# Kernel tuning notes

Hardware: AMD Instinct MI355X
Metric: run time of the kernel (lower is better)

The kernel has to match this reference:

```python
import jax, jax.numpy as jnp
import numpy as np

OUT, IN = 5632, 2048
GROUP_SIZE = 128
N_GROUPS = (OUT * IN) // GROUP_SIZE
LORA_SCALE = 32.0 / 16.0  # lora_alpha / lora_r


def dequantize_int4(packed, scales, zeros):
    # packed: [numel//2], each byte holds two 4-bit codes (low nibble first)
    low = packed & 0xF
    high = (packed >> 4) & 0xF
    q = jnp.stack([low, high], axis=-1).reshape(-1).astype(jnp.float32)  # [numel]
    q = q.reshape(N_GROUPS, GROUP_SIZE)
    w = (q - zeros[:, None]) * scales[:, None]
    return w.reshape(OUT, IN)


def setup_inputs() -> dict:
    key = jax.random.key(0)
    k1, k2, k3, k4, k5, k6 = jax.random.split(key, 6)
    x = jax.random.normal(k1, (4, 2048, IN), dtype=jnp.float32)
    packed = jax.random.randint(k2, ((OUT * IN) // 2,), 0, 256, dtype=jnp.int32)
    scales = jax.random.uniform(k3, (N_GROUPS,), dtype=jnp.float32) * 0.02 + 1e-3
    zeros = jax.random.uniform(k4, (N_GROUPS,), dtype=jnp.float32) * 15.0
    lora_A = jax.random.normal(k5, (IN, 16), dtype=jnp.float32) * (1.0 / np.sqrt(IN))
    lora_B = jax.random.normal(k6, (16, OUT), dtype=jnp.float32) * 0.02
    return {"x": x, "packed": packed, "scales": scales, "zeros": zeros,
            "lora_A": lora_A, "lora_B": lora_B}


def reference(x, packed, scales, zeros, lora_A, lora_B):
    W = dequantize_int4(packed, scales, zeros)            # [OUT, IN]
    base = jnp.einsum('bsi,oi->bso', x, W)                # F.linear(x, W)
    lora = ((x @ lora_A) @ lora_B) * LORA_SCALE           # low-rank path
    return base + lora
```

## Files before the change

### kernel.cpp

```cpp
#include <hip/hip_runtime.h>

#define M_DIM 8192
#define K_DIM 2048
#define N_DIM 5632

typedef __attribute__((ext_vector_type(8))) short short8;
typedef __attribute__((ext_vector_type(4))) short s4v;
typedef __attribute__((ext_vector_type(4))) float f32x4;

__device__ __forceinline__ short f2b(float f) {
  union { float f; unsigned u; } v; v.f = f;
  unsigned r = v.u + 0x7FFFu + ((v.u >> 16) & 1u);
  return (short)(r >> 16);
}

__device__ __forceinline__ void async16(void* lds, const void* g) {
  __builtin_amdgcn_global_load_lds(
      (const __attribute__((address_space(1))) unsigned*)g,
      (__attribute__((address_space(3))) unsigned*)lds,
      16, 0, 0);
}

__global__ __launch_bounds__(256) void cvt_x_kernel(const float* __restrict__ x,
                                                    short* __restrict__ xb) {
  long t = (long)blockIdx.x * 256 + threadIdx.x;
  float4 f = ((const float4*)x)[t];
  s4v o;
  o[0] = f2b(f.x); o[1] = f2b(f.y); o[2] = f2b(f.z); o[3] = f2b(f.w);
  *(s4v*)(xb + 4 * t) = o;
}

__global__ __launch_bounds__(256) void lat_kernel(const float* __restrict__ lA,
                                                  float* __restrict__ lAT) {
  int i = blockIdx.x * 256 + threadIdx.x;
  const float4* row = (const float4*)(lA + (size_t)i * 16);
  float4 v0 = row[0], v1 = row[1], v2 = row[2], v3 = row[3];
  float vals[16] = {v0.x, v0.y, v0.z, v0.w, v1.x, v1.y, v1.z, v1.w,
                    v2.x, v2.y, v2.z, v2.w, v3.x, v3.y, v3.z, v3.w};
#pragma unroll
  for (int r = 0; r < 16; ++r) lAT[r * K_DIM + i] = vals[r] * 2.0f;
}

__global__ __launch_bounds__(256) void dequant_lora_kernel(
    const int* __restrict__ packed, const float* __restrict__ scales,
    const float* __restrict__ zeros, const float* __restrict__ lAT,
    const float* __restrict__ lB, short* __restrict__ wb) {
  int o = blockIdx.x;
  int i0 = threadIdx.x * 8;
  long e0 = (long)o * K_DIM + i0;
  int4 p = ((const int4*)packed)[e0 >> 3];
  int g = (int)(e0 >> 7);
  float s = scales[g], z = zeros[g];

  float accv[8];
#pragma unroll
  for (int d = 0; d < 4; ++d) {
    int pv = (&p.x)[d];
    accv[2 * d]     = ((float)(pv & 0xF) - z) * s;
    accv[2 * d + 1] = ((float)((pv >> 4) & 0xF) - z) * s;
  }
#pragma unroll
  for (int r = 0; r < 16; ++r) {
    float b = lB[r * N_DIM + o];
    const float4* ar = (const float4*)&lAT[r * K_DIM + i0];
    float4 a0 = ar[0], a1 = ar[1];
    accv[0] += a0.x * b; accv[1] += a0.y * b;
    accv[2] += a0.z * b; accv[3] += a0.w * b;
    accv[4] += a1.x * b; accv[5] += a1.y * b;
    accv[6] += a1.z * b; accv[7] += a1.w * b;
  }
  short8 out8;
#pragma unroll
  for (int j = 0; j < 8; ++j) out8[j] = f2b(accv[j]);
  *(short8*)(wb + e0) = out8;
}

__global__ __launch_bounds__(512, 2) void gemm_kernel(const short* __restrict__ xb,
                                                      const short* __restrict__ wb,
                                                      float* __restrict__ out) {
  __shared__ __align__(16) short lds[65536];

  const int tid = threadIdx.x;
  const int lane = tid & 63;
  const int wave = tid >> 6;
  const int wm = wave >> 2, wn = wave & 3;
  const int l15 = lane & 15, quad = lane >> 4;

  int flat = blockIdx.x;
  int swz = (flat & 7) * 88 + (flat >> 3);
  int bm = swz / 22, bn = swz - bm * 22;
  const int m0 = bm * 256, n0 = bn * 256;

  const short* a_base = xb + (size_t)m0 * K_DIM;
  const short* b_base = wb + (size_t)n0 * K_DIM;

  const int rswz = quad ^ ((l15 >> 1) & 3);
  const int a_rd = (wm * 128 + l15) * 32 + rswz * 8;
  const int b_rd = 32768 + (wn * 64 + l15) * 32 + rswz * 8;

  const int srow = tid >> 2;
  const int schunk = (tid & 3) ^ ((srow >> 1) & 3);
  const short* ag0 = a_base + (size_t)srow * K_DIM + schunk * 8;
  const short* ag1 = ag0 + (size_t)128 * K_DIM;
  const short* bg0 = b_base + (size_t)srow * K_DIM + schunk * 8;
  const short* bg1 = bg0 + (size_t)128 * K_DIM;
  const int sl0 = tid * 8, sl1 = (512 + tid) * 8;

  f32x4 acc[8][4] = {};
  short8 bfA[4], af1A[4], bfB[4], af1B[4];

#pragma unroll
  for (int t = 0; t < 3; ++t) {
    const int sb = t * 8192;
    async16(&lds[sb + sl0], ag0 + t * 32);
    async16(&lds[sb + sl1], ag1 + t * 32);
    async16(&lds[32768 + sb + sl0], bg0 + t * 32);
    async16(&lds[32768 + sb + sl1], bg1 + t * 32);
  }
  asm volatile("s_waitcnt vmcnt(4)" ::: "memory");
  __builtin_amdgcn_s_barrier();
#pragma unroll
  for (int ni = 0; ni < 4; ++ni) bfA[ni] = *(const short8*)&lds[b_rd + ni * 512];
#pragma unroll
  for (int mi = 0; mi < 4; ++mi) af1A[mi] = *(const short8*)&lds[a_rd + mi * 512];

  auto tile = [&](int k, short8* bfc, short8* af1c, short8* bfn, short8* af1n,
                  bool do_stage, bool do_pref) {
    const int bo = (k & 3) * 8192;
    const int no_ = ((k + 1) & 3) * 8192;
    const int so = ((k + 3) & 3) * 8192;
    short8 af2[4];
#pragma unroll
    for (int mi = 0; mi < 4; ++mi)
      af2[mi] = *(const short8*)&lds[bo + a_rd + (4 + mi) * 512];
    if (do_pref) {
#pragma unroll
      for (int ni = 0; ni < 4; ++ni)
        bfn[ni] = *(const short8*)&lds[no_ + b_rd + ni * 512];
#pragma unroll
      for (int mi = 0; mi < 4; ++mi)
        af1n[mi] = *(const short8*)&lds[no_ + a_rd + mi * 512];
    }
    if (do_stage) {
      async16(&lds[so + sl0], ag0 + (k + 3) * 32);
      async16(&lds[so + sl1], ag1 + (k + 3) * 32);
      async16(&lds[32768 + so + sl0], bg0 + (k + 3) * 32);
      async16(&lds[32768 + so + sl1], bg1 + (k + 3) * 32);
    }
    __builtin_amdgcn_s_setprio(1);
#pragma unroll
    for (int mi = 0; mi < 4; ++mi)
#pragma unroll
      for (int ni = 0; ni < 4; ++ni)
        acc[mi][ni] = __builtin_amdgcn_mfma_f32_16x16x32_bf16(
            af1c[mi], bfc[ni], acc[mi][ni], 0, 0, 0);
#pragma unroll
    for (int mi = 0; mi < 4; ++mi)
#pragma unroll
      for (int ni = 0; ni < 4; ++ni)
        acc[4 + mi][ni] = __builtin_amdgcn_mfma_f32_16x16x32_bf16(
            af2[mi], bfc[ni], acc[4 + mi][ni], 0, 0, 0);
    __builtin_amdgcn_s_setprio(0);
  };

#pragma unroll 1
  for (int k = 0; k < 60; k += 2) {
    tile(k, bfA, af1A, bfB, af1B, true, true);
    asm volatile("s_waitcnt vmcnt(4)" ::: "memory");
    __builtin_amdgcn_s_barrier();
    tile(k + 1, bfB, af1B, bfA, af1A, true, true);
    asm volatile("s_waitcnt vmcnt(4)" ::: "memory");
    __builtin_amdgcn_s_barrier();
  }
  tile(60, bfA, af1A, bfB, af1B, true, true);
  asm volatile("s_waitcnt vmcnt(4)" ::: "memory");
  __builtin_amdgcn_s_barrier();
  tile(61, bfB, af1B, bfA, af1A, false, true);
  asm volatile("s_waitcnt vmcnt(0)" ::: "memory");
  __builtin_amdgcn_s_barrier();
  tile(62, bfA, af1A, bfB, af1B, false, true);
  tile(63, bfB, af1B, bfA, af1A, false, false);

  float* op = out + (size_t)(m0 + wm * 128 + quad * 4) * N_DIM + n0 + wn * 64 + l15;
#pragma unroll
  for (int mi = 0; mi < 8; ++mi)
#pragma unroll
    for (int r = 0; r < 4; ++r)
#pragma unroll
      for (int ni = 0; ni < 4; ++ni)
        op[(size_t)(mi * 16 + r) * N_DIM + ni * 16] = acc[mi][ni][r];
}

extern "C" void kernel_launch(void* const* d_in, const int* in_sizes, int n_in,
                              void* d_out, int out_size, void* d_ws, size_t ws_size,
                              hipStream_t stream) {
  const float* x      = (const float*)d_in[0];
  const int*   packed = (const int*)d_in[1];
  const float* scales = (const float*)d_in[2];
  const float* zeros  = (const float*)d_in[3];
  const float* lA     = (const float*)d_in[4];
  const float* lB     = (const float*)d_in[5];
  float* out = (float*)d_out;

  short* xb = (short*)d_ws;
  short* wb = xb + (size_t)M_DIM * K_DIM;
  float* lAT = out + ((size_t)4 * 2048 * N_DIM - 16 * K_DIM);

  cvt_x_kernel<<<(M_DIM * K_DIM) / (256 * 4), 256, 0, stream>>>(x, xb);
  lat_kernel<<<K_DIM / 256, 256, 0, stream>>>(lA, lAT);
  dequant_lora_kernel<<<N_DIM, 256, 0, stream>>>(packed, scales, zeros, lAT, lB, wb);
  gemm_kernel<<<dim3(N_DIM / 256 * (M_DIM / 256)), 512, 0, stream>>>(xb, wb, out);
}
```

Measured before the change: 456.9 us.

## Split GEMM k-tile into four barrier-separated phases with interleaved fragment loads

```diff
diff --git a/kernel.cpp b/kernel.cpp
--- a/kernel.cpp
+++ b/kernel.cpp
@@ -88,8 +88,8 @@
 
   int flat = blockIdx.x;
   int swz = (flat & 7) * 88 + (flat >> 3);
-  int bm = swz / 22, bn = swz - bm * 22;
-  const int m0 = bm * 256, n0 = bn * 256;
+  int bm = swz / 22, bn_ = swz - bm * 22;
+  const int m0 = bm * 256, n0 = bn_ * 256;
 
   const short* a_base = xb + (size_t)m0 * K_DIM;
   const short* b_base = wb + (size_t)n0 * K_DIM;
@@ -107,7 +107,7 @@
   const int sl0 = tid * 8, sl1 = (512 + tid) * 8;
 
   f32x4 acc[8][4] = {};
-  short8 bfA[4], af1A[4], bfB[4], af1B[4];
+  short8 bfA[4], bfB[4], aX[2], aY[2];
 
 #pragma unroll
   for (int t = 0; t < 3; ++t) {
@@ -121,65 +121,81 @@
   __builtin_amdgcn_s_barrier();
 #pragma unroll
   for (int ni = 0; ni < 4; ++ni) bfA[ni] = *(const short8*)&lds[b_rd + ni * 512];
-#pragma unroll
-  for (int mi = 0; mi < 4; ++mi) af1A[mi] = *(const short8*)&lds[a_rd + mi * 512];
-
-  auto tile = [&](int k, short8* bfc, short8* af1c, short8* bfn, short8* af1n,
-                  bool do_stage, bool do_pref) {
+  aX[0] = *(const short8*)&lds[a_rd];
+  aX[1] = *(const short8*)&lds[a_rd + 512];
+
+  auto tile = [&](int k, short8* bc, short8* bnx, bool do_stage, bool do_next,
+                  int vm) {
     const int bo = (k & 3) * 8192;
     const int no_ = ((k + 1) & 3) * 8192;
     const int so = ((k + 3) & 3) * 8192;
-    short8 af2[4];
-#pragma unroll
-    for (int mi = 0; mi < 4; ++mi)
-      af2[mi] = *(const short8*)&lds[bo + a_rd + (4 + mi) * 512];
-    if (do_pref) {
-#pragma unroll
-      for (int ni = 0; ni < 4; ++ni)
-        bfn[ni] = *(const short8*)&lds[no_ + b_rd + ni * 512];
-#pragma unroll
-      for (int mi = 0; mi < 4; ++mi)
-        af1n[mi] = *(const short8*)&lds[no_ + a_rd + mi * 512];
-    }
-    if (do_stage) {
-      async16(&lds[so + sl0], ag0 + (k + 3) * 32);
-      async16(&lds[so + sl1], ag1 + (k + 3) * 32);
-      async16(&lds[32768 + so + sl0], bg0 + (k + 3) * 32);
-      async16(&lds[32768 + so + sl1], bg1 + (k + 3) * 32);
-    }
-    __builtin_amdgcn_s_setprio(1);
-#pragma unroll
-    for (int mi = 0; mi < 4; ++mi)
-#pragma unroll
-      for (int ni = 0; ni < 4; ++ni)
-        acc[mi][ni] = __builtin_amdgcn_mfma_f32_16x16x32_bf16(
-            af1c[mi], bfc[ni], acc[mi][ni], 0, 0, 0);
-#pragma unroll
-    for (int mi = 0; mi < 4; ++mi)
-#pragma unroll
-      for (int ni = 0; ni < 4; ++ni)
-        acc[4 + mi][ni] = __builtin_amdgcn_mfma_f32_16x16x32_bf16(
-            af2[mi], bfc[ni], acc[4 + mi][ni], 0, 0, 0);
-    __builtin_amdgcn_s_setprio(0);
+    aY[0] = *(const short8*)&lds[bo + a_rd + 2 * 512];
+    aY[1] = *(const short8*)&lds[bo + a_rd + 3 * 512];
+    if (do_stage) async16(&lds[so + sl0], ag0 + (k + 3) * 32);
+    __builtin_amdgcn_s_setprio(1);
+#pragma unroll
+    for (int ni = 0; ni < 4; ++ni) {
+      acc[0][ni] = __builtin_amdgcn_mfma_f32_16x16x32_bf16(aX[0], bc[ni], acc[0][ni], 0, 0, 0);
+      acc[1][ni] = __builtin_amdgcn_mfma_f32_16x16x32_bf16(aX[1], bc[ni], acc[1][ni], 0, 0, 0);
+    }
+    __builtin_amdgcn_s_setprio(0);
+    __builtin_amdgcn_s_barrier();
+    aX[0] = *(const short8*)&lds[bo + a_rd + 4 * 512];
+    aX[1] = *(const short8*)&lds[bo + a_rd + 5 * 512];
+    if (do_next) {
+      bnx[0] = *(const short8*)&lds[no_ + b_rd];
+      bnx[1] = *(const short8*)&lds[no_ + b_rd + 512];
+    }
+    if (do_stage) async16(&lds[so + sl1], ag1 + (k + 3) * 32);
+    __builtin_amdgcn_s_setprio(1);
+#pragma unroll
+    for (int ni = 0; ni < 4; ++ni) {
+      acc[2][ni] = __builtin_amdgcn_mfma_f32_16x16x32_bf16(aY[0], bc[ni], acc[2][ni], 0, 0, 0);
+      acc[3][ni] = __builtin_amdgcn_mfma_f32_16x16x32_bf16(aY[1], bc[ni], acc[3][ni], 0, 0, 0);
+    }
+    __builtin_amdgcn_s_setprio(0);
+    __builtin_amdgcn_s_barrier();
+    aY[0] = *(const short8*)&lds[bo + a_rd + 6 * 512];
+    aY[1] = *(const short8*)&lds[bo + a_rd + 7 * 512];
+    if (do_next) {
+      bnx[2] = *(const short8*)&lds[no_ + b_rd + 2 * 512];
+      bnx[3] = *(const short8*)&lds[no_ + b_rd + 3 * 512];
+    }
+    if (do_stage) async16(&lds[32768 + so + sl0], bg0 + (k + 3) * 32);
+    __builtin_amdgcn_s_setprio(1);
+#pragma unroll
+    for (int ni = 0; ni < 4; ++ni) {
+      acc[4][ni] = __builtin_amdgcn_mfma_f32_16x16x32_bf16(aX[0], bc[ni], acc[4][ni], 0, 0, 0);
+      acc[5][ni] = __builtin_amdgcn_mfma_f32_16x16x32_bf16(aX[1], bc[ni], acc[5][ni], 0, 0, 0);
+    }
+    __builtin_amdgcn_s_setprio(0);
+    __builtin_amdgcn_s_barrier();
+    if (do_next) {
+      aX[0] = *(const short8*)&lds[no_ + a_rd];
+      aX[1] = *(const short8*)&lds[no_ + a_rd + 512];
+    }
+    if (do_stage) async16(&lds[32768 + so + sl1], bg1 + (k + 3) * 32);
+    __builtin_amdgcn_s_setprio(1);
+#pragma unroll
+    for (int ni = 0; ni < 4; ++ni) {
+      acc[6][ni] = __builtin_amdgcn_mfma_f32_16x16x32_bf16(aY[0], bc[ni], acc[6][ni], 0, 0, 0);
+      acc[7][ni] = __builtin_amdgcn_mfma_f32_16x16x32_bf16(aY[1], bc[ni], acc[7][ni], 0, 0, 0);
+    }
+    __builtin_amdgcn_s_setprio(0);
+    if (vm == 4) asm volatile("s_waitcnt vmcnt(4)" ::: "memory");
+    else if (vm == 0) asm volatile("s_waitcnt vmcnt(0)" ::: "memory");
+    __builtin_amdgcn_s_barrier();
   };
 
 #pragma unroll 1
   for (int k = 0; k < 60; k += 2) {
-    tile(k, bfA, af1A, bfB, af1B, true, true);
-    asm volatile("s_waitcnt vmcnt(4)" ::: "memory");
-    __builtin_amdgcn_s_barrier();
-    tile(k + 1, bfB, af1B, bfA, af1A, true, true);
-    asm volatile("s_waitcnt vmcnt(4)" ::: "memory");
-    __builtin_amdgcn_s_barrier();
-  }
-  tile(60, bfA, af1A, bfB, af1B, true, true);
-  asm volatile("s_waitcnt vmcnt(4)" ::: "memory");
-  __builtin_amdgcn_s_barrier();
-  tile(61, bfB, af1B, bfA, af1A, false, true);
-  asm volatile("s_waitcnt vmcnt(0)" ::: "memory");
-  __builtin_amdgcn_s_barrier();
-  tile(62, bfA, af1A, bfB, af1B, false, true);
-  tile(63, bfB, af1B, bfA, af1A, false, false);
+    tile(k,     bfA, bfB, true, true, 4);
+    tile(k + 1, bfB, bfA, true, true, 4);
+  }
+  tile(60, bfA, bfB, true,  true, 4);
+  tile(61, bfB, bfA, false, true, 0);
+  tile(62, bfA, bfB, false, true, -1);
+  tile(63, bfB, bfA, false, false, -1);
 
   float* op = out + (size_t)(m0 + wm * 128 + quad * 4) * N_DIM + n0 + wn * 64 + l15;
 #pragma unroll
@@ -188,7 +204,8 @@
     for (int r = 0; r < 4; ++r)
 #pragma unroll
       for (int ni = 0; ni < 4; ++ni)
-        op[(size_t)(mi * 16 + r) * N_DIM + ni * 16] = acc[mi][ni][r];
+        __builtin_nontemporal_store(acc[mi][ni][r],
+                                    &op[(size_t)(mi * 16 + r) * N_DIM + ni * 16]);
 }
 
 extern "C" void kernel_launch(void* const* d_in, const int* in_sizes, int n_in,
```

Result: no change. 455.6 us (-0.3%).

## Restructure GEMM main loop into double-buffered half-tile stages with staggered A/B loads

Applied to the files above, without the earlier changes.

```diff
diff --git a/kernel.cpp b/kernel.cpp
--- a/kernel.cpp
+++ b/kernel.cpp
@@ -88,98 +88,111 @@
 
   int flat = blockIdx.x;
   int swz = (flat & 7) * 88 + (flat >> 3);
-  int bm = swz / 22, bn = swz - bm * 22;
-  const int m0 = bm * 256, n0 = bn * 256;
+  int bm = swz / 22, bn_ = swz - bm * 22;
+  const int m0 = bm * 256, n0 = bn_ * 256;
 
   const short* a_base = xb + (size_t)m0 * K_DIM;
   const short* b_base = wb + (size_t)n0 * K_DIM;
 
-  const int rswz = quad ^ ((l15 >> 1) & 3);
-  const int a_rd = (wm * 128 + l15) * 32 + rswz * 8;
-  const int b_rd = 32768 + (wn * 64 + l15) * 32 + rswz * 8;
-
-  const int srow = tid >> 2;
-  const int schunk = (tid & 3) ^ ((srow >> 1) & 3);
-  const short* ag0 = a_base + (size_t)srow * K_DIM + schunk * 8;
-  const short* ag1 = ag0 + (size_t)128 * K_DIM;
-  const short* bg0 = b_base + (size_t)srow * K_DIM + schunk * 8;
-  const short* bg1 = bg0 + (size_t)128 * K_DIM;
+  const int a_rd = (wm * 128 + l15) * 32 + quad * 8;
+  const int b_rd = (wn * 64 + l15) * 32 + quad * 8;
+
+  const short* ag0 = a_base + (size_t)(tid >> 2) * K_DIM + (tid & 3) * 8;
+  const short* bg0 = b_base + (size_t)(tid >> 2) * K_DIM + (tid & 3) * 8;
   const int sl0 = tid * 8, sl1 = (512 + tid) * 8;
 
   f32x4 acc[8][4] = {};
-  short8 bfA[4], af1A[4], bfB[4], af1B[4];
-
-#pragma unroll
-  for (int t = 0; t < 3; ++t) {
-    const int sb = t * 8192;
-    async16(&lds[sb + sl0], ag0 + t * 32);
-    async16(&lds[sb + sl1], ag1 + t * 32);
-    async16(&lds[32768 + sb + sl0], bg0 + t * 32);
-    async16(&lds[32768 + sb + sl1], bg1 + t * 32);
-  }
+
+  auto stageA = [&](int t, int s) {
+    const int d = (t & 1) * 16384 + s * 8192;
+    const short* g = ag0 + t * 64 + s * 32;
+    async16(&lds[d + sl0], g);
+    async16(&lds[d + sl1], g + (size_t)128 * K_DIM);
+  };
+  auto stageB = [&](int t, int s) {
+    const int d = 32768 + (t & 1) * 16384 + s * 8192;
+    const short* g = bg0 + t * 64 + s * 32;
+    async16(&lds[d + sl0], g);
+    async16(&lds[d + sl1], g + (size_t)128 * K_DIM);
+  };
+
+  stageA(0, 0); stageB(0, 0);
+  stageA(0, 1); stageB(0, 1);
   asm volatile("s_waitcnt vmcnt(4)" ::: "memory");
   __builtin_amdgcn_s_barrier();
-#pragma unroll
-  for (int ni = 0; ni < 4; ++ni) bfA[ni] = *(const short8*)&lds[b_rd + ni * 512];
-#pragma unroll
-  for (int mi = 0; mi < 4; ++mi) af1A[mi] = *(const short8*)&lds[a_rd + mi * 512];
-
-  auto tile = [&](int k, short8* bfc, short8* af1c, short8* bfn, short8* af1n,
-                  bool do_stage, bool do_pref) {
-    const int bo = (k & 3) * 8192;
-    const int no_ = ((k + 1) & 3) * 8192;
-    const int so = ((k + 3) & 3) * 8192;
-    short8 af2[4];
-#pragma unroll
-    for (int mi = 0; mi < 4; ++mi)
-      af2[mi] = *(const short8*)&lds[bo + a_rd + (4 + mi) * 512];
-    if (do_pref) {
-#pragma unroll
-      for (int ni = 0; ni < 4; ++ni)
-        bfn[ni] = *(const short8*)&lds[no_ + b_rd + ni * 512];
-#pragma unroll
-      for (int mi = 0; mi < 4; ++mi)
-        af1n[mi] = *(const short8*)&lds[no_ + a_rd + mi * 512];
-    }
-    if (do_stage) {
-      async16(&lds[so + sl0], ag0 + (k + 3) * 32);
-      async16(&lds[so + sl1], ag1 + (k + 3) * 32);
-      async16(&lds[32768 + so + sl0], bg0 + (k + 3) * 32);
-      async16(&lds[32768 + so + sl1], bg1 + (k + 3) * 32);
-    }
-    __builtin_amdgcn_s_setprio(1);
-#pragma unroll
-    for (int mi = 0; mi < 4; ++mi)
-#pragma unroll
-      for (int ni = 0; ni < 4; ++ni)
-        acc[mi][ni] = __builtin_amdgcn_mfma_f32_16x16x32_bf16(
-            af1c[mi], bfc[ni], acc[mi][ni], 0, 0, 0);
-#pragma unroll
-    for (int mi = 0; mi < 4; ++mi)
-#pragma unroll
-      for (int ni = 0; ni < 4; ++ni)
-        acc[4 + mi][ni] = __builtin_amdgcn_mfma_f32_16x16x32_bf16(
-            af2[mi], bfc[ni], acc[4 + mi][ni], 0, 0, 0);
-    __builtin_amdgcn_s_setprio(0);
+
+  auto tile = [&](int t, bool st, int vm1, int vm3) {
+    const int cb = (t & 1) * 16384;
+    short8 af[4], bf[4];
+#pragma unroll
+    for (int n = 0; n < 4; ++n) bf[n] = *(const short8*)&lds[32768 + cb + b_rd + n * 512];
+#pragma unroll
+    for (int m = 0; m < 4; ++m) af[m] = *(const short8*)&lds[cb + a_rd + m * 512];
+    if (st) stageA(t + 1, 0);
+    __builtin_amdgcn_s_barrier();
+    asm volatile("s_waitcnt lgkmcnt(0)" ::: "memory");
+    __builtin_amdgcn_sched_barrier(0);
+    __builtin_amdgcn_s_setprio(1);
+#pragma unroll
+    for (int m = 0; m < 4; ++m)
+#pragma unroll
+      for (int n = 0; n < 4; ++n)
+        acc[m][n] = __builtin_amdgcn_mfma_f32_16x16x32_bf16(af[m], bf[n], acc[m][n], 0, 0, 0);
+    __builtin_amdgcn_s_setprio(0);
+    __builtin_amdgcn_s_barrier();
+#pragma unroll
+    for (int m = 0; m < 4; ++m) af[m] = *(const short8*)&lds[cb + a_rd + (4 + m) * 512];
+    if (st) stageB(t + 1, 0);
+    __builtin_amdgcn_s_barrier();
+    asm volatile("s_waitcnt lgkmcnt(0)" ::: "memory");
+    __builtin_amdgcn_sched_barrier(0);
+    __builtin_amdgcn_s_setprio(1);
+#pragma unroll
+    for (int m = 0; m < 4; ++m)
+#pragma unroll
+      for (int n = 0; n < 4; ++n)
+        acc[4 + m][n] = __builtin_amdgcn_mfma_f32_16x16x32_bf16(af[m], bf[n], acc[4 + m][n], 0, 0, 0);
+    __builtin_amdgcn_s_setprio(0);
+    if (vm1 == 4) asm volatile("s_waitcnt vmcnt(4)" ::: "memory");
+    else if (vm1 == 0) asm volatile("s_waitcnt vmcnt(0)" ::: "memory");
+    __builtin_amdgcn_s_barrier();
+#pragma unroll
+    for (int n = 0; n < 4; ++n) bf[n] = *(const short8*)&lds[32768 + cb + 8192 + b_rd + n * 512];
+#pragma unroll
+    for (int m = 0; m < 4; ++m) af[m] = *(const short8*)&lds[cb + 8192 + a_rd + m * 512];
+    if (st) stageA(t + 1, 1);
+    __builtin_amdgcn_s_barrier();
+    asm volatile("s_waitcnt lgkmcnt(0)" ::: "memory");
+    __builtin_amdgcn_sched_barrier(0);
+    __builtin_amdgcn_s_setprio(1);
+#pragma unroll
+    for (int m = 0; m < 4; ++m)
+#pragma unroll
+      for (int n = 0; n < 4; ++n)
+        acc[m][n] = __builtin_amdgcn_mfma_f32_16x16x32_bf16(af[m], bf[n], acc[m][n], 0, 0, 0);
+    __builtin_amdgcn_s_setprio(0);
+    __builtin_amdgcn_s_barrier();
+#pragma unroll
+    for (int m = 0; m < 4; ++m) af[m] = *(const short8*)&lds[cb + 8192 + a_rd + (4 + m) * 512];
+    if (st) stageB(t + 1, 1);
+    __builtin_amdgcn_s_barrier();
+    asm volatile("s_waitcnt lgkmcnt(0)" ::: "memory");
+    __builtin_amdgcn_sched_barrier(0);
+    __builtin_amdgcn_s_setprio(1);
+#pragma unroll
+    for (int m = 0; m < 4; ++m)
+#pragma unroll
+      for (int n = 0; n < 4; ++n)
+        acc[4 + m][n] = __builtin_amdgcn_mfma_f32_16x16x32_bf16(af[m], bf[n], acc[4 + m][n], 0, 0, 0);
+    __builtin_amdgcn_s_setprio(0);
+    if (vm3 == 4) asm volatile("s_waitcnt vmcnt(4)" ::: "memory");
+    else if (vm3 == 0) asm volatile("s_waitcnt vmcnt(0)" ::: "memory");
+    __builtin_amdgcn_s_barrier();
   };
 
 #pragma unroll 1
-  for (int k = 0; k < 60; k += 2) {
-    tile(k, bfA, af1A, bfB, af1B, true, true);
-    asm volatile("s_waitcnt vmcnt(4)" ::: "memory");
-    __builtin_amdgcn_s_barrier();
-    tile(k + 1, bfB, af1B, bfA, af1A, true, true);
-    asm volatile("s_waitcnt vmcnt(4)" ::: "memory");
-    __builtin_amdgcn_s_barrier();
-  }
-  tile(60, bfA, af1A, bfB, af1B, true, true);
-  asm volatile("s_waitcnt vmcnt(4)" ::: "memory");
-  __builtin_amdgcn_s_barrier();
-  tile(61, bfB, af1B, bfA, af1A, false, true);
-  asm volatile("s_waitcnt vmcnt(0)" ::: "memory");
-  __builtin_amdgcn_s_barrier();
-  tile(62, bfA, af1A, bfB, af1B, false, true);
-  tile(63, bfB, af1B, bfA, af1A, false, false);
+  for (int t = 0; t < 31; ++t) tile(t, true, 4, 4);
+  tile(31, false, 0, -1);
 
   float* op = out + (size_t)(m0 + wm * 128 + quad * 4) * N_DIM + n0 + wn * 64 + l15;
 #pragma unroll
```

Result: slower. 466.3 us (+2.1%).
